# Kernel optimization log

Measured on AMD Instinct MI355X. Metric: run time of the kernel, lower is better.

Reference implementation:

```python
import jax, jax.numpy as jnp
import numpy as np
import math

# real<->complex packing matching the module's _c2r/_r2c (trailing dim 2)
def _r2c(x):
    return x[..., 0] + 1j * x[..., 1]

H, N, CH, RANK, LMAX = 256, 64, 1, 1, 2048


def setup_inputs() -> dict:
    key = jax.random.key(0)
    k0, k1, k2, k3, k4, k5 = jax.random.split(key, 6)
    C = jax.random.normal(k0, (CH, H, N, 2), jnp.float32)
    B = jax.random.normal(k1, (1, H, N, 2), jnp.float32)
    P = 0.3 * jax.random.normal(k2, (RANK, H, N, 2), jnp.float32)
    # w must have negative real part (Hurwitz) so Cauchy denominators stay away from zero
    w_re = -(jnp.abs(jax.random.normal(k3, (H, N))) * 0.5 + 0.1)
    w_im = jnp.pi * jax.random.normal(k4, (H, N))
    w = jnp.stack([w_re, w_im], axis=-1).astype(jnp.float32)
    log_dt = jax.random.uniform(k5, (H,), jnp.float32,
                                math.log(1e-3), math.log(1e-1))
    return {"C": C, "B": B, "P": P, "w": w, "log_dt": log_dt, "L": LMAX}


def reference(C, B, P, w, log_dt, L):
    Cc = _r2c(C)            # (c, H, N) complex
    Bc = _r2c(B)            # (1, H, N)
    Pc = _r2c(P)            # (r, H, N)
    wc = _r2c(w)            # (H, N)
    Qc = jnp.conj(Pc)       # Q = P.conj() (resolve_conj path)
    dt = jnp.exp(log_dt)    # (H,)

    # FFT nodes + bilinear transform (rate == 1.0)
    F = L // 2 + 1
    omega = jnp.exp(-2j * jnp.pi / L) ** jnp.arange(F)   # (F,) complex64
    z = 2 * (1 - omega) / (1 + omega)                     # (F,)

    w_dt = wc * dt[:, None].astype(wc.dtype)              # (H, N)

    Bcat = jnp.concatenate([Bc, Pc], axis=0)              # (1+r, H, N)
    Ccat = jnp.concatenate([Cc, Qc], axis=0)              # (c+r, H, N)
    v = Bcat[:, None] * Ccat[None]                        # (1+r, c+r, H, N)

    # Cauchy kernel: r[a,b,h,f] = sum_n v[a,b,h,n] / (z[f] - w_dt[h,n])
    denom = z - w_dt[..., None]                           # (H, N, F)
    r = jnp.sum(v[..., None] / denom, axis=-2)            # (1+r, c+r, H, F)
    r = r * dt[None, None, :, None].astype(r.dtype)

    # rank-1 Woodbury low-rank correction
    k_f = r[:-1, :-1] - r[:-1, -1:] * r[-1:, :-1] / (1 + r[-1:, -1:])  # (1, c, H, F)
    k_f = k_f * 2 / (1 + omega)

    k = jnp.fft.irfft(k_f, n=L, axis=-1)[..., :L]         # (1, c, H, L) real
    k_B = k[-1]                                           # (c, H, L)
    return k_B
```

## Files before the change

### kernel.cpp

```cpp
#include <hip/hip_runtime.h>


typedef float v2f __attribute__((ext_vector_type(2)));

#define HH 256
#define NN 64
#define LL 2048
#define MM 1024
#define NT 256
#define FPT 4

#define PI_OVER_1024 0.0030679615757712823f
#define PI_OVER_512  0.0061359231515425647f

__global__ __launch_bounds__(NT) void ssk_fused(
    const float* __restrict__ Cin, const float* __restrict__ Bin,
    const float* __restrict__ Pin, const float* __restrict__ Win,
    const float* __restrict__ logdt, float* __restrict__ out)
{
    __shared__ float4 sD4[NN * 3];
    __shared__ float2 sX[MM + 1];
    __shared__ float2 sA[MM];
    __shared__ float2 sBf[MM];

    const int h = blockIdx.x;
    const int t = threadIdx.x;
    const float dtv = __expf(logdt[h]);

    if (t < NN) {
        const int base = (h * NN + t) * 2;
        const float Br = Bin[base], Bi = Bin[base + 1];
        const float Cr = Cin[base], Ci = Cin[base + 1];
        const float Pr = Pin[base], Pi = Pin[base + 1];
        const float v00r = Br * Cr - Bi * Ci, v00i = Br * Ci + Bi * Cr;
        sD4[t * 3 + 0] = make_float4(Win[base] * dtv, Win[base + 1] * dtv, v00r, v00i);
        sD4[t * 3 + 1] = make_float4(Br * Pr + Bi * Pi, Bi * Pr - Br * Pi,
                                     Pr * Cr - Pi * Ci, Pr * Ci + Pi * Cr);
        sD4[t * 3 + 2] = make_float4(Pr * Pr + Pi * Pi, 0.f, 0.f, 0.f);
        float r = v00r;
        #pragma unroll
        for (int off = 32; off; off >>= 1) r += __shfl_xor(r, off, 64);
        if (t == 0) sX[MM] = make_float2(0.5f * dtv * r, 0.f);
    }
    __syncthreads();

    {
        const float* sDf = (const float*)sD4;
        v2f u[FPT], t1[FPT];
        v2f s00[FPT], s01[FPT], s10[FPT], s11[FPT];
        #pragma unroll
        for (int rep = 0; rep < FPT; ++rep) {
            const int f = t + rep * NT;
            float si, co;
            __sincosf(PI_OVER_1024 * (float)f, &si, &co);
            u[rep]  = (v2f){1.0f + co, -si};
            t1[rep] = (v2f){2.0f * (1.0f - co), 2.0f * si};
            s00[rep] = (v2f){0.f, 0.f}; s01[rep] = (v2f){0.f, 0.f};
            s10[rep] = (v2f){0.f, 0.f}; s11[rep] = (v2f){0.f, 0.f};
        }
        #pragma unroll 4
        for (int n = 0; n < NN; ++n) {
            const float4 q0 = sD4[n * 3 + 0];
            const float4 q1 = sD4[n * 3 + 1];
            const float v11 = sDf[n * 12 + 8];
            #pragma unroll
            for (int rep = 0; rep < FPT; ++rep) {
                v2f den = t1[rep];
                den = den - (v2f){q0.x, q0.x} * u[rep];
                den = den + (v2f){q0.y, q0.y} * (v2f){u[rep].y, -u[rep].x};
                const float inv = __builtin_amdgcn_rcpf(den.x * den.x + den.y * den.y);
                const v2f e  = den * (v2f){inv, -inv};
                const v2f es = {e.y, e.x};
                s00[rep] = s00[rep] + (v2f){q0.z, q0.z} * e;
                s00[rep] = s00[rep] + (v2f){-q0.w, q0.w} * es;
                s01[rep] = s01[rep] + (v2f){q1.x, q1.x} * e;
                s01[rep] = s01[rep] + (v2f){-q1.y, q1.y} * es;
                s10[rep] = s10[rep] + (v2f){q1.z, q1.z} * e;
                s10[rep] = s10[rep] + (v2f){-q1.w, q1.w} * es;
                s11[rep] = s11[rep] + (v2f){v11, v11} * e;
            }
        }
        #pragma unroll
        for (int rep = 0; rep < FPT; ++rep) {
            const int f = t + rep * NT;
            const float gr = dtv * u[rep].x, gi = dtv * u[rep].y;
            const float numr = s01[rep].x * s10[rep].x - s01[rep].y * s10[rep].y;
            const float numi = s01[rep].x * s10[rep].y + s01[rep].y * s10[rep].x;
            const float qr = 1.0f + (gr * s11[rep].x - gi * s11[rep].y);
            const float qi = gr * s11[rep].y + gi * s11[rep].x;
            const float tr = gr * numr - gi * numi;
            const float ti = gr * numi + gi * numr;
            const float qinv = __builtin_amdgcn_rcpf(qr * qr + qi * qi);
            const float cr = (tr * qr + ti * qi) * qinv;
            const float ci = (ti * qr - tr * qi) * qinv;
            const float kr = 2.0f * dtv * (s00[rep].x - cr);
            float       ki = 2.0f * dtv * (s00[rep].y - ci);
            if (f == 0) ki = 0.0f;
            sX[f] = make_float2(kr, ki);
        }
    }
    __syncthreads();

    const float HS = 4.8828125e-4f;
    #pragma unroll
    for (int rep = 0; rep < FPT; ++rep) {
        const int f = t + rep * NT;
        const float2 a1 = sX[f];
        const float2 x2 = sX[MM - f];
        const float er  = HS * (a1.x + x2.x), eim = HS * (a1.y - x2.y);
        const float gr  = HS * (a1.x - x2.x), gim = HS * (a1.y + x2.y);
        float st, ct;
        __sincosf(PI_OVER_1024 * (float)f, &st, &ct);
        const float Or = ct * gr - st * gim;
        const float Oi = ct * gim + st * gr;
        sA[f] = make_float2(er - Oi, eim + Or);
    }
    __syncthreads();

    float2* cur = sA;
    float2* nxt = sBf;
    #pragma unroll
    for (int i = 0; i < 10; ++i) {
        const int s = 1 << i;
        #pragma unroll
        for (int half = 0; half < 2; ++half) {
            const int b = t + half * NT;
            const int j = b & ~(s - 1);
            const float2 a = cur[b];
            const float2 c = cur[b + 512];
            const float sr = a.x + c.x, sim = a.y + c.y;
            const float dr = a.x - c.x, dim = a.y - c.y;
            float st, ct;
            __sincosf(PI_OVER_512 * (float)j, &st, &ct);
            nxt[b + j]     = make_float2(sr, sim);
            nxt[b + j + s] = make_float2(ct * dr - st * dim, ct * dim + st * dr);
        }
        __syncthreads();
        float2* tmp = cur; cur = nxt; nxt = tmp;
    }

    float2* outv = (float2*)(out + (size_t)h * LL);
    #pragma unroll
    for (int rep = 0; rep < FPT; ++rep) {
        const int m = t + rep * NT;
        outv[m] = cur[m];
    }
}

extern "C" void kernel_launch(void* const* d_in, const int* in_sizes, int n_in,
                              void* d_out, int out_size, void* d_ws, size_t ws_size,
                              hipStream_t stream) {
    const float* C  = (const float*)d_in[0];
    const float* B  = (const float*)d_in[1];
    const float* P  = (const float*)d_in[2];
    const float* W  = (const float*)d_in[3];
    const float* ld = (const float*)d_in[4];
    float* out = (float*)d_out;
    ssk_fused<<<HH, NT, 0, stream>>>(C, B, P, W, ld, out);
}
```

Measured before the change: 75.24 us.

## Replace radix-2 Stockham FFT with radix-4 stages fused with post-processing

The inverse FFT changes from ten radix-2 Stockham stages to five radix-4 stages. The first radix-4 stage is fused into the real-to-complex post-processing loop, which removes one shared-memory round trip. Fewer stages means fewer __syncthreads barriers and fewer shared-memory passes, and twiddles for w^2 and w^3 come from double-angle identities instead of extra sincos calls. The output store is widened to float4. The cost is higher register pressure per thread, and the radix-4 indexing and twiddle signs must match the original transform direction.

```diff
diff --git a/kernel.cpp b/kernel.cpp
--- a/kernel.cpp
+++ b/kernel.cpp
@@ -102,48 +102,77 @@
     __syncthreads();
 
     const float HS = 4.8828125e-4f;
+    float2* cur;
+    float2* nxt;
+    {
+        const int b = t;
+        float2 Z[4];
+        #pragma unroll
+        for (int r = 0; r < 4; ++r) {
+            const int f = b + r * 256;
+            const float2 a1 = sX[f];
+            const float2 x2 = sX[MM - f];
+            const float er  = HS * (a1.x + x2.x), eim = HS * (a1.y - x2.y);
+            const float gr  = HS * (a1.x - x2.x), gim = HS * (a1.y + x2.y);
+            float st, ct;
+            __sincosf(PI_OVER_1024 * (float)f, &st, &ct);
+            Z[r] = make_float2(er - (ct * gim + st * gr), eim + (ct * gr - st * gim));
+        }
+        const float2 T0 = {Z[0].x + Z[2].x, Z[0].y + Z[2].y};
+        const float2 T1 = {Z[1].x + Z[3].x, Z[1].y + Z[3].y};
+        const float2 T2 = {Z[0].x - Z[2].x, Z[0].y - Z[2].y};
+        const float2 D3 = {Z[1].x - Z[3].x, Z[1].y - Z[3].y};
+        const float2 T3 = {-D3.y, D3.x};
+        float s1, c1;
+        __sincosf(PI_OVER_512 * (float)b, &s1, &c1);
+        const float c2 = 1.f - 2.f * s1 * s1, s2 = 2.f * s1 * c1;
+        const float c3 = c1 * c2 - s1 * s2,  s3 = s1 * c2 + c1 * s2;
+        const float2 A0 = {T0.x + T1.x, T0.y + T1.y};
+        const float2 A1 = {T2.x + T3.x, T2.y + T3.y};
+        const float2 A2 = {T0.x - T1.x, T0.y - T1.y};
+        const float2 A3 = {T2.x - T3.x, T2.y - T3.y};
+        sBf[4 * b + 0] = A0;
+        sBf[4 * b + 1] = make_float2(c1 * A1.x - s1 * A1.y, c1 * A1.y + s1 * A1.x);
+        sBf[4 * b + 2] = make_float2(c2 * A2.x - s2 * A2.y, c2 * A2.y + s2 * A2.x);
+        sBf[4 * b + 3] = make_float2(c3 * A3.x - s3 * A3.y, c3 * A3.y + s3 * A3.x);
+        cur = sBf; nxt = sA;
+        __syncthreads();
+    }
+
     #pragma unroll
-    for (int rep = 0; rep < FPT; ++rep) {
-        const int f = t + rep * NT;
-        const float2 a1 = sX[f];
-        const float2 x2 = sX[MM - f];
-        const float er  = HS * (a1.x + x2.x), eim = HS * (a1.y - x2.y);
-        const float gr  = HS * (a1.x - x2.x), gim = HS * (a1.y + x2.y);
-        float st, ct;
-        __sincosf(PI_OVER_1024 * (float)f, &st, &ct);
-        const float Or = ct * gr - st * gim;
-        const float Oi = ct * gim + st * gr;
-        sA[f] = make_float2(er - Oi, eim + Or);
-    }
-    __syncthreads();
-
-    float2* cur = sA;
-    float2* nxt = sBf;
-    #pragma unroll
-    for (int i = 0; i < 10; ++i) {
-        const int s = 1 << i;
-        #pragma unroll
-        for (int half = 0; half < 2; ++half) {
-            const int b = t + half * NT;
-            const int j = b & ~(s - 1);
-            const float2 a = cur[b];
-            const float2 c = cur[b + 512];
-            const float sr = a.x + c.x, sim = a.y + c.y;
-            const float dr = a.x - c.x, dim = a.y - c.y;
-            float st, ct;
-            __sincosf(PI_OVER_512 * (float)j, &st, &ct);
-            nxt[b + j]     = make_float2(sr, sim);
-            nxt[b + j + s] = make_float2(ct * dr - st * dim, ct * dim + st * dr);
-        }
+    for (int i = 1; i < 5; ++i) {
+        const int s = 1 << (2 * i);
+        const int b = t;
+        const int j = b & ~(s - 1);
+        const float2 X0 = cur[b], X1 = cur[b + 256], X2 = cur[b + 512], X3 = cur[b + 768];
+        const float2 T0 = {X0.x + X2.x, X0.y + X2.y};
+        const float2 T1 = {X1.x + X3.x, X1.y + X3.y};
+        const float2 T2 = {X0.x - X2.x, X0.y - X2.y};
+        const float2 D3 = {X1.x - X3.x, X1.y - X3.y};
+        const float2 T3 = {-D3.y, D3.x};
+        float s1, c1;
+        __sincosf(PI_OVER_512 * (float)j, &s1, &c1);
+        const float c2 = 1.f - 2.f * s1 * s1, s2 = 2.f * s1 * c1;
+        const float c3 = c1 * c2 - s1 * s2,  s3 = s1 * c2 + c1 * s2;
+        const int o = b + 3 * j;
+        const float2 A0 = {T0.x + T1.x, T0.y + T1.y};
+        const float2 A1 = {T2.x + T3.x, T2.y + T3.y};
+        const float2 A2 = {T0.x - T1.x, T0.y - T1.y};
+        const float2 A3 = {T2.x - T3.x, T2.y - T3.y};
+        nxt[o]         = A0;
+        nxt[o + s]     = make_float2(c1 * A1.x - s1 * A1.y, c1 * A1.y + s1 * A1.x);
+        nxt[o + 2 * s] = make_float2(c2 * A2.x - s2 * A2.y, c2 * A2.y + s2 * A2.x);
+        nxt[o + 3 * s] = make_float2(c3 * A3.x - s3 * A3.y, c3 * A3.y + s3 * A3.x);
         __syncthreads();
         float2* tmp = cur; cur = nxt; nxt = tmp;
     }
 
-    float2* outv = (float2*)(out + (size_t)h * LL);
+    float4* outv4 = (float4*)(out + (size_t)h * LL);
     #pragma unroll
-    for (int rep = 0; rep < FPT; ++rep) {
+    for (int rep = 0; rep < 2; ++rep) {
         const int m = t + rep * NT;
-        outv[m] = cur[m];
+        const float2 z0 = cur[2 * m], z1 = cur[2 * m + 1];
+        outv4[m] = make_float4(z0.x, z0.y, z1.x, z1.y);
     }
 }
 
```

Result: no change. 75.01 us (-0.3%).
